# Kernel optimization log

Hardware: AMD Instinct MI355X
Metric: run time of the kernel (lower is better)

Reference implementation:

```python
import jax, jax.numpy as jnp
import numpy as np

N, E, H, C = 100000, 1600000, 4, 32  # nodes, edges, heads, per-head channels
F_IN, F_HID, F_OUT = 128, 32, 16
NEG_SLOPE = 0.2


def setup_inputs() -> dict:
    key = jax.random.key(0)
    ks = jax.random.split(key, 16)
    s = 0.05
    return {
        "x": jax.random.normal(ks[0], (N, F_IN), jnp.float32),
        "edge_index": jax.random.randint(ks[1], (2, E), 0, N, jnp.int32),
        "W0": jax.random.normal(ks[2], (F_IN, H * C), jnp.float32) * s,
        "att_src0": jax.random.normal(ks[3], (H, C), jnp.float32) * s,
        "att_dst0": jax.random.normal(ks[4], (H, C), jnp.float32) * s,
        "b0": jax.random.normal(ks[5], (H * C,), jnp.float32) * s,
        "W1": jax.random.normal(ks[6], (H * C, H * C), jnp.float32) * s,
        "att_src1": jax.random.normal(ks[7], (H, C), jnp.float32) * s,
        "att_dst1": jax.random.normal(ks[8], (H, C), jnp.float32) * s,
        "b1": jax.random.normal(ks[9], (H * C,), jnp.float32) * s,
        "Wm1": jax.random.normal(ks[10], (H * C, F_HID), jnp.float32) * s,
        "bm1": jax.random.normal(ks[11], (F_HID,), jnp.float32) * s,
        "Wm2": jax.random.normal(ks[12], (F_HID, F_OUT), jnp.float32) * s,
        "bm2": jax.random.normal(ks[13], (F_OUT,), jnp.float32) * s,
    }


def gat_layer(x, src, dst, W, att_src, att_dst, bias):
    n = x.shape[0]
    h = (x @ W).reshape(n, H, C)                       # [N,H,C]
    a_src = jnp.einsum("nhc,hc->nh", h, att_src)       # [N,H]
    a_dst = jnp.einsum("nhc,hc->nh", h, att_dst)       # [N,H]
    e = a_src[src] + a_dst[dst]                        # [E,H]
    e = jnp.where(e > 0, e, NEG_SLOPE * e)             # leaky_relu(0.2)
    m = jax.ops.segment_max(e, dst, num_segments=n)    # [N,H] segment softmax
    ee = jnp.exp(e - m[dst])
    z = jax.ops.segment_sum(ee, dst, num_segments=n)
    alpha = ee / z[dst]                                # [E,H]
    msg = alpha[:, :, None] * h[src]                   # [E,H,C]
    out = jax.ops.segment_sum(msg, dst, num_segments=n)  # [N,H,C]
    return out.reshape(n, H * C) + bias


def reference(x, edge_index, W0, att_src0, att_dst0, b0,
              W1, att_src1, att_dst1, b1, Wm1, bm1, Wm2, bm2):
    src, dst = edge_index[0], edge_index[1]
    x = jax.nn.relu(gat_layer(x, src, dst, W0, att_src0, att_dst0, b0))
    x = jax.nn.relu(gat_layer(x, src, dst, W1, att_src1, att_dst1, b1))
    x = jax.nn.relu(x @ Wm1 + bm1)
    return x @ Wm2 + bm2
```

## Files before the change

### kernel.cpp

```cpp
#include <hip/hip_runtime.h>
#include <hip/hip_bf16.h>

#define NEG 0.2f

typedef __attribute__((ext_vector_type(8))) short short8v;
typedef __attribute__((ext_vector_type(4))) float f32x4;

static __device__ __forceinline__ float bf2f(unsigned int u16){
  return __uint_as_float(u16 << 16);
}
static __device__ __forceinline__ unsigned short f2bf(float f){
  __hip_bfloat16 h = __float2bfloat16(f);
  return *reinterpret_cast<unsigned short*>(&h);
}

#define CHUNK 2048
#define PER_T 8


static __device__ __forceinline__ void bcount_body(
    const int* __restrict__ dst, int* __restrict__ bcnt, int E, int NB,
    int blk, int* lc)
{
  int t = threadIdx.x;
  int ebase = blk * CHUNK;
  for (int j=t; j<NB; j+=256) lc[j]=0;
  __syncthreads();
  #pragma unroll
  for (int k=0;k<PER_T;++k){
    int i = ebase + t + k*256;
    if (i < E) atomicAdd(&lc[dst[i] >> 8], 1);
  }
  __syncthreads();
  for (int j=t; j<NB; j+=256){
    int c = lc[j];
    if (c) atomicAdd(&bcnt[j], c);
  }
}

static __device__ __forceinline__ void binpass_body(
    const int* __restrict__ src, const int* __restrict__ dst,
    int* __restrict__ bfill, unsigned int* __restrict__ pairs, int E, int NB,
    int blk, int* lcnt, int* lbase)
{
  int t = threadIdx.x;
  int ebase = blk * CHUNK;
  for (int j=t; j<NB; j+=256) lcnt[j]=0;
  __syncthreads();
  unsigned int pv[PER_T]; int pb[PER_T];
  #pragma unroll
  for (int k=0;k<PER_T;++k){
    int i = ebase + t + k*256;
    pb[k] = -1;
    if (i < E){
      int d = dst[i];
      int s = src[i];
      pb[k] = d >> 8;
      pv[k] = ((unsigned int)s << 8) | (unsigned int)(d & 255);
      atomicAdd(&lcnt[pb[k]], 1);
    }
  }
  __syncthreads();
  for (int j=t; j<NB; j+=256){
    int c = lcnt[j];
    lbase[j] = c ? atomicAdd(&bfill[j], c) : 0;
    lcnt[j] = 0;
  }
  __syncthreads();
  #pragma unroll
  for (int k=0;k<PER_T;++k){
    if (pb[k] >= 0){
      int ofs = atomicAdd(&lcnt[pb[k]], 1);
      pairs[lbase[pb[k]] + ofs] = pv[k];
    }
  }
}

template<int IN_BF16>
static __device__ __forceinline__ void gemm_att_body(
    const void* __restrict__ xin_, const unsigned short* __restrict__ wt,
    const float* __restrict__ atts, const float* __restrict__ attd,
    unsigned short* __restrict__ hb, float* __restrict__ as_, float* __restrict__ ad_,
    int n, int blk, unsigned short* xls)
{
  int t = threadIdx.x;
  int base = blk*64;
  int nrem = n - base;
  if (IN_BF16){
    const uint4* Xb = reinterpret_cast<const uint4*>(xin_);
    #pragma unroll
    for (int j=0;j<4;++j){
      int i = t + j*256;
      int row = i >> 4, c16 = i & 15;
      uint4 v = (row < nrem) ? Xb[(size_t)(base+row)*16 + c16]
                             : make_uint4(0,0,0,0);
      int addr = row*256 + ((c16*16) ^ ((row&7)<<4));
      *reinterpret_cast<uint4*>(reinterpret_cast<char*>(xls) + addr) = v;
    }
  } else {
    const float4* X4 = reinterpret_cast<const float4*>(xin_);
    #pragma unroll
    for (int j=0;j<8;++j){
      int i = t + j*256;
      int row = i >> 5, cb = i & 31;
      float4 v = (row < nrem) ? X4[(size_t)(base+row)*32 + cb] : make_float4(0.f,0.f,0.f,0.f);
      unsigned int p0 = (unsigned int)f2bf(v.x) | ((unsigned int)f2bf(v.y)<<16);
      unsigned int p1 = (unsigned int)f2bf(v.z) | ((unsigned int)f2bf(v.w)<<16);
      int addr = row*256 + ((cb*8) ^ ((row&7)<<4));
      *reinterpret_cast<uint2*>(reinterpret_cast<char*>(xls) + addr) = make_uint2(p0,p1);
    }
  }
  __syncthreads();
  int w = t >> 6;
  int l = t & 63;
  int l15 = l & 15, l4 = l >> 4;
  int n0 = w*32;
  short8v bfr[2][4];
  #pragma unroll
  for (int nt=0;nt<2;++nt){
    const unsigned short* bp = wt + (size_t)(n0 + nt*16 + l15)*128 + l4*8;
    #pragma unroll
    for (int kk=0;kk<4;++kk)
      bfr[nt][kk] = *reinterpret_cast<const short8v*>(bp + kk*32);
  }
  f32x4 acc[4][2];
  #pragma unroll
  for (int mt=0;mt<4;++mt)
    #pragma unroll
    for (int nt=0;nt<2;++nt)
      acc[mt][nt] = (f32x4){0.f,0.f,0.f,0.f};
  #pragma unroll
  for (int kk=0;kk<4;++kk){
    short8v afr[4];
    #pragma unroll
    for (int mt=0;mt<4;++mt){
      int row = mt*16 + l15;
      int addr = row*256 + ((kk*64 + l4*16) ^ ((row&7)<<4));
      afr[mt] = *reinterpret_cast<const short8v*>(reinterpret_cast<char*>(xls) + addr);
    }
    #pragma unroll
    for (int mt=0;mt<4;++mt)
      #pragma unroll
      for (int nt=0;nt<2;++nt)
        acc[mt][nt] = __builtin_amdgcn_mfma_f32_16x16x32_bf16(afr[mt], bfr[nt][kk], acc[mt][nt], 0, 0, 0);
  }
  float av0 = atts[n0 + l15],    av1 = atts[n0 + 16 + l15];
  float dv0 = attd[n0 + l15],    dv1 = attd[n0 + 16 + l15];
  #pragma unroll
  for (int mt=0;mt<4;++mt){
    #pragma unroll
    for (int r=0;r<4;++r){
      float ps = acc[mt][0][r]*av0 + acc[mt][1][r]*av1;
      float pd = acc[mt][0][r]*dv0 + acc[mt][1][r]*dv1;
      ps += __shfl_xor(ps,1); ps += __shfl_xor(ps,2);
      ps += __shfl_xor(ps,4); ps += __shfl_xor(ps,8);
      pd += __shfl_xor(pd,1); pd += __shfl_xor(pd,2);
      pd += __shfl_xor(pd,4); pd += __shfl_xor(pd,8);
      int node = base + mt*16 + l4*4 + r;
      if (l15==0 && node < n){
        as_[node*4 + w] = ps;
        ad_[node*4 + w] = pd;
      }
    }
  }
  __syncthreads();
  #pragma unroll
  for (int mt=0;mt<4;++mt)
    #pragma unroll
    for (int nt=0;nt<2;++nt)
      #pragma unroll
      for (int r=0;r<4;++r){
        int row = mt*16 + l4*4 + r;
        int col = n0 + nt*16 + l15;
        xls[row*128 + col] = f2bf(acc[mt][nt][r]);
      }
  __syncthreads();
  const uint4* xsrc = reinterpret_cast<const uint4*>(xls);
  uint4* hdst = reinterpret_cast<uint4*>(hb + (size_t)base*128);
  #pragma unroll
  for (int j=0;j<4;++j){
    int i = t + j*256;
    int row = i >> 4;
    if (row < nrem) hdst[i] = xsrc[i];
  }
}


__global__ __launch_bounds__(256) void k_wconv_bcount(
    const float* __restrict__ W0, const float* __restrict__ W1,
    unsigned short* __restrict__ wt0, unsigned short* __restrict__ wt1,
    const int* __restrict__ dst, int* __restrict__ bcnt, int E, int NB)
{
  __shared__ int lc[512];
  int b = blockIdx.x;
  if (b < 128){
    const float* W = (b < 64) ? W0 : W1;
    unsigned short* wt = (b < 64) ? wt0 : wt1;
    int i = (b & 63)*256 + threadIdx.x;
    int k = i >> 7, nn = i & 127;
    wt[nn*128 + k] = f2bf(W[i]);
  } else {
    bcount_body(dst, bcnt, E, NB, b - 128, lc);
  }
}

__global__ __launch_bounds__(256) void k_bscan(
    const int* __restrict__ bcnt, int* __restrict__ bstart,
    int* __restrict__ bfill, int NB)
{
  __shared__ int sd[256];
  int t = threadIdx.x;
  int i0 = 2*t, i1 = 2*t+1;
  int v0 = (i0<NB) ? bcnt[i0] : 0;
  int v1 = (i1<NB) ? bcnt[i1] : 0;
  int s = v0+v1;
  sd[t]=s; __syncthreads();
  for (int off=1; off<256; off<<=1){
    int x = (t>=off) ? sd[t-off] : 0;
    __syncthreads();
    sd[t] += x;
    __syncthreads();
  }
  int ex = sd[t]-s;
  if (i0<=NB){ bstart[i0]=ex; if(i0<NB) bfill[i0]=ex; }
  ex += v0;
  if (i1<=NB){ bstart[i1]=ex; if(i1<NB) bfill[i1]=ex; }
}

__global__ __launch_bounds__(256) void k_gemm1_binpass(
    const float* __restrict__ xin, const unsigned short* __restrict__ wt,
    const float* __restrict__ atts, const float* __restrict__ attd,
    unsigned short* __restrict__ hb, float* __restrict__ as_, float* __restrict__ ad_,
    int n, int nBin,
    const int* __restrict__ src, const int* __restrict__ dst,
    int* __restrict__ bfill, unsigned int* __restrict__ pairs, int E, int NB)
{
  __shared__ __align__(16) unsigned short xls[64*128];
  __shared__ int lcnt[512];
  __shared__ int lbase[512];
  int b = blockIdx.x;
  if (b < nBin){
    binpass_body(src, dst, bfill, pairs, E, NB, b, lcnt, lbase);
  } else {
    gemm_att_body<0>(xin, wt, atts, attd, hb, as_, ad_, n, b - nBin, xls);
  }
}

__global__ __launch_bounds__(256) void k_gemm2(
    const unsigned short* __restrict__ xin, const unsigned short* __restrict__ wt,
    const float* __restrict__ atts, const float* __restrict__ attd,
    unsigned short* __restrict__ hb, float* __restrict__ as_, float* __restrict__ ad_, int n)
{
  __shared__ __align__(16) unsigned short xls[64*128];
  gemm_att_body<1>(xin, wt, atts, attd, hb, as_, ad_, n, blockIdx.x, xls);
}

__global__ __launch_bounds__(256) void k_csr(
    const unsigned int* __restrict__ pairs, const int* __restrict__ bstart,
    int* __restrict__ rowptr, int* __restrict__ csr, int n)
{
  __shared__ int lc[256];
  __shared__ int sd[256];
  __shared__ int rp[257];
  int b = blockIdx.x;
  int base = b << 8;
  int t = threadIdx.x;
  int cnt = n - base; if (cnt > 256) cnt = 256;
  int beg = bstart[b], end = bstart[b+1];
  lc[t]=0; __syncthreads();
  for (int i = beg + t; i < end; i += 256)
    atomicAdd(&lc[pairs[i] & 255u], 1);
  __syncthreads();
  int v = lc[t];
  sd[t]=v; __syncthreads();
  for (int off=1; off<256; off<<=1){
    int x = (t>=off) ? sd[t-off] : 0;
    __syncthreads();
    sd[t] += x;
    __syncthreads();
  }
  rp[t+1] = beg + sd[t];
  if (t==0) rp[0] = beg;
  lc[t] = 0;
  __syncthreads();
  if (t < cnt) rowptr[base + t] = rp[t];
  if (t==0 && base + cnt == n) rowptr[n] = rp[cnt];
  for (int i = beg + t; i < end; i += 256){
    unsigned int p = pairs[i];
    int d = (int)(p & 255u);
    int ofs = atomicAdd(&lc[d], 1);
    csr[rp[d] + ofs] = (int)(p >> 8);
  }
}

__global__ __launch_bounds__(256) void k_aggr(
    const unsigned short* __restrict__ hb, const float* __restrict__ as_,
    const float* __restrict__ ad_, const int* __restrict__ rowptr,
    const int* __restrict__ csr, const float* __restrict__ bias,
    unsigned short* __restrict__ out, int n)
{
  int wid = (int)((blockIdx.x*(size_t)blockDim.x + threadIdx.x) >> 6);
  int lane = threadIdx.x & 63;
  if (wid >= n) return;
  int half = lane >> 5;
  int li   = lane & 31;
  int c0   = li*4;
  int head = li >> 3;
  const uint2* __restrict__ h2 = reinterpret_cast<const uint2*>(hb);
  float adn = ad_[wid*4 + head];
  int beg = rowptr[wid], end = rowptr[wid+1];
  int deg = end - beg;
  float4 acc = make_float4(0.f,0.f,0.f,0.f);
  float z = 0.f;
  int nfull = deg & ~7;
  int lim = beg + nfull;
  int i = beg + half*4;
  int s0=0,s1=0,s2=0,s3=0;
  if (i < lim){ s0=csr[i]; s1=csr[i+1]; s2=csr[i+2]; s3=csr[i+3]; }
  for (; i < lim; ){
    int ni = i + 8;
    int t0=0,t1=0,t2=0,t3=0;
    if (ni < lim){ t0=csr[ni]; t1=csr[ni+1]; t2=csr[ni+2]; t3=csr[ni+3]; }
    float e0 = as_[s0*4+head];
    float e1 = as_[s1*4+head];
    float e2 = as_[s2*4+head];
    float e3 = as_[s3*4+head];
    uint2 p0 = h2[s0*32 + li];
    uint2 p1 = h2[s1*32 + li];
    uint2 p2 = h2[s2*32 + li];
    uint2 p3 = h2[s3*32 + li];
    e0 += adn; e1 += adn; e2 += adn; e3 += adn;
    e0 = (e0>0.f)?e0:NEG*e0;
    e1 = (e1>0.f)?e1:NEG*e1;
    e2 = (e2>0.f)?e2:NEG*e2;
    e3 = (e3>0.f)?e3:NEG*e3;
    float x0 = __expf(e0);
    float x1 = __expf(e1);
    float x2 = __expf(e2);
    float x3 = __expf(e3);
    z += (x0+x1)+(x2+x3);
    acc.x = fmaf(x0, bf2f(p0.x & 0xffffu), acc.x);
    acc.y = fmaf(x0, bf2f(p0.x >> 16),     acc.y);
    acc.z = fmaf(x0, bf2f(p0.y & 0xffffu), acc.z);
    acc.w = fmaf(x0, bf2f(p0.y >> 16),     acc.w);
    acc.x = fmaf(x1, bf2f(p1.x & 0xffffu), acc.x);
    acc.y = fmaf(x1, bf2f(p1.x >> 16),     acc.y);
    acc.z = fmaf(x1, bf2f(p1.y & 0xffffu), acc.z);
    acc.w = fmaf(x1, bf2f(p1.y >> 16),     acc.w);
    acc.x = fmaf(x2, bf2f(p2.x & 0xffffu), acc.x);
    acc.y = fmaf(x2, bf2f(p2.x >> 16),     acc.y);
    acc.z = fmaf(x2, bf2f(p2.y & 0xffffu), acc.z);
    acc.w = fmaf(x2, bf2f(p2.y >> 16),     acc.w);
    acc.x = fmaf(x3, bf2f(p3.x & 0xffffu), acc.x);
    acc.y = fmaf(x3, bf2f(p3.x >> 16),     acc.y);
    acc.z = fmaf(x3, bf2f(p3.y & 0xffffu), acc.z);
    acc.w = fmaf(x3, bf2f(p3.y >> 16),     acc.w);
    i = ni; s0=t0; s1=t1; s2=t2; s3=t3;
  }
  for (int j = beg + nfull + half; j < end; j += 2){
    int s = csr[j];
    float e = as_[s*4+head] + adn;
    e = (e>0.f)?e:NEG*e;
    float ee = __expf(e);
    z += ee;
    uint2 pv = h2[s*32 + li];
    acc.x = fmaf(ee, bf2f(pv.x & 0xffffu), acc.x);
    acc.y = fmaf(ee, bf2f(pv.x >> 16),     acc.y);
    acc.z = fmaf(ee, bf2f(pv.y & 0xffffu), acc.z);
    acc.w = fmaf(ee, bf2f(pv.y >> 16),     acc.w);
  }
  z     += __shfl_xor(z, 32);
  acc.x += __shfl_xor(acc.x, 32);
  acc.y += __shfl_xor(acc.y, 32);
  acc.z += __shfl_xor(acc.z, 32);
  acc.w += __shfl_xor(acc.w, 32);
  if (half == 0){
    float4 o;
    if (deg > 0){
      float rz = 1.f/z;
      o.x = fmaxf(fmaf(acc.x,rz,bias[c0  ]), 0.f);
      o.y = fmaxf(fmaf(acc.y,rz,bias[c0+1]), 0.f);
      o.z = fmaxf(fmaf(acc.z,rz,bias[c0+2]), 0.f);
      o.w = fmaxf(fmaf(acc.w,rz,bias[c0+3]), 0.f);
    } else {
      o.x = fmaxf(bias[c0  ], 0.f);
      o.y = fmaxf(bias[c0+1], 0.f);
      o.z = fmaxf(bias[c0+2], 0.f);
      o.w = fmaxf(bias[c0+3], 0.f);
    }
    unsigned int lo = (unsigned int)f2bf(o.x) | ((unsigned int)f2bf(o.y)<<16);
    unsigned int hi = (unsigned int)f2bf(o.z) | ((unsigned int)f2bf(o.w)<<16);
    *reinterpret_cast<uint2*>(out + (size_t)wid*128 + c0) = make_uint2(lo,hi);
  }
}

__global__ __launch_bounds__(256) void k_mlp(
    const unsigned short* __restrict__ xb, const float* __restrict__ Wm1, const float* __restrict__ bm1,
    const float* __restrict__ Wm2, const float* __restrict__ bm2,
    float* __restrict__ out, int n)
{
  __shared__ float xs[64*129];
  __shared__ float w1s[128*32];
  __shared__ float hs[64*33];
  __shared__ float w2s[32*16];
  __shared__ float b1s[32];
  __shared__ float b2s[16];
  int t = threadIdx.x;
  int base = blockIdx.x*64;
  const uint4* Xb = reinterpret_cast<const uint4*>(xb);
  #pragma unroll
  for (int j=0;j<4;++j){
    int i = t + j*256;
    int row = i >> 4, seg = i & 15;
    uint4 v = (base+row < n) ? Xb[(size_t)(base+row)*16 + seg] : make_uint4(0,0,0,0);
    float* xp = &xs[row*129 + seg*8];
    xp[0] = bf2f(v.x & 0xffffu); xp[1] = bf2f(v.x >> 16);
    xp[2] = bf2f(v.y & 0xffffu); xp[3] = bf2f(v.y >> 16);
    xp[4] = bf2f(v.z & 0xffffu); xp[5] = bf2f(v.z >> 16);
    xp[6] = bf2f(v.w & 0xffffu); xp[7] = bf2f(v.w >> 16);
  }
  for (int i=t; i<128*32; i+=256) w1s[i]=Wm1[i];
  for (int i=t; i<32*16;  i+=256) w2s[i]=Wm2[i];
  if (t<32) b1s[t]=bm1[t];
  if (t<16) b2s[t]=bm2[t];
  __syncthreads();
  int l = t&63, g = t>>6;
  float hid[8];
  #pragma unroll
  for (int j=0;j<8;++j) hid[j]=0.f;
  for (int k=0;k<128;++k){
    float xk = xs[l*129+k];
    #pragma unroll
    for (int j=0;j<8;++j) hid[j] = fmaf(xk, w1s[k*32 + g*8 + j], hid[j]);
  }
  #pragma unroll
  for (int j=0;j<8;++j) hs[l*33 + g*8 + j] = fmaxf(hid[j] + b1s[g*8+j], 0.f);
  __syncthreads();
  float o[4] = {0.f,0.f,0.f,0.f};
  for (int k=0;k<32;++k){
    float xv = hs[l*33+k];
    #pragma unroll
    for (int j=0;j<4;++j) o[j] = fmaf(xv, w2s[k*16 + g*4 + j], o[j]);
  }
  int node = base + l;
  if (node < n){
    #pragma unroll
    for (int j=0;j<4;++j) out[(size_t)node*16 + g*4 + j] = o[j] + b2s[g*4+j];
  }
}

extern "C" void kernel_launch(void* const* d_in, const int* in_sizes, int n_in,
                              void* d_out, int out_size, void* d_ws, size_t ws_size,
                              hipStream_t stream)
{
  const float* x   = (const float*)d_in[0];
  const int*   ei  = (const int*)  d_in[1];
  const float* W0  = (const float*)d_in[2];
  const float* as0 = (const float*)d_in[3];
  const float* ad0 = (const float*)d_in[4];
  const float* b0  = (const float*)d_in[5];
  const float* W1  = (const float*)d_in[6];
  const float* as1 = (const float*)d_in[7];
  const float* ad1 = (const float*)d_in[8];
  const float* b1  = (const float*)d_in[9];
  const float* Wm1 = (const float*)d_in[10];
  const float* bm1 = (const float*)d_in[11];
  const float* Wm2 = (const float*)d_in[12];
  const float* bm2 = (const float*)d_in[13];
  int N = in_sizes[0]/128;
  int E = in_sizes[1]/2;
  const int* srcI = ei;
  const int* dstI = ei + E;

  char* ws = (char*)d_ws;
  size_t off = 0;
  auto alloc = [&](size_t bytes)->void*{
    void* p = ws + off; off += (bytes + 255) & ~(size_t)255; return p;
  };
  unsigned short* hbuf = (unsigned short*)alloc((size_t)N*128*2);
  unsigned short* xbuf = (unsigned short*)alloc((size_t)N*128*2);
  float* asb   = (float*)alloc((size_t)N*4*4);
  float* adb   = (float*)alloc((size_t)N*4*4);
  int* rowptr  = (int*)alloc((size_t)(N+1)*4);
  int* bcnt    = (int*)alloc(2048);
  int* bstart  = (int*)alloc(2052);
  int* bfill   = (int*)alloc(2048);
  int* csr     = (int*)alloc((size_t)E*4);
  unsigned int* pairs = (unsigned int*)alloc((size_t)E*4);
  unsigned short* wt0 = (unsigned short*)alloc(128*128*2);
  unsigned short* wt1 = (unsigned short*)alloc(128*128*2);
  (void)ws_size; (void)n_in; (void)out_size;

  int NB = (N + 255) >> 8;
  int gC = (E + CHUNK - 1) / CHUNK;
  int gG = (N+63)/64;
  int gA = (int)(((size_t)N*64 + 255)/256);

  hipMemsetAsync(bcnt, 0, 2048, stream);
  k_wconv_bcount<<<128+gC,256,0,stream>>>(W0, W1, wt0, wt1, dstI, bcnt, E, NB);
  k_bscan       <<<1,256,0,stream>>>(bcnt, bstart, bfill, NB);
  k_gemm1_binpass<<<gG+gC,256,0,stream>>>(x, wt0, as0, ad0, hbuf, asb, adb, N, gC,
                                          srcI, dstI, bfill, pairs, E, NB);
  k_csr         <<<NB,256,0,stream>>>(pairs, bstart, rowptr, csr, N);
  k_aggr        <<<gA,256,0,stream>>>(hbuf, asb, adb, rowptr, csr, b0, xbuf, N);
  k_gemm2       <<<gG,256,0,stream>>>(xbuf, wt1, as1, ad1, hbuf, asb, adb, N);
  k_aggr        <<<gA,256,0,stream>>>(hbuf, asb, adb, rowptr, csr, b1, xbuf, N);
  k_mlp         <<<gG,256,0,stream>>>(xbuf, Wm1, bm1, Wm2, bm2, (float*)d_out, N);
}
```

Before: 294.5 us.

## Fuse bin scan into count kernel, use half-wave per node in aggregation

The bin-count kernel now has its last-finishing block, found through an atomic done counter, run the exclusive scan. This removes the separate single-block scan launch. The aggregation kernel maps one 32-lane group per node instead of a full 64-lane wave split into halves, which drops the cross-half shuffle reduction and the idle half-wave on low-degree nodes. Row pointers are stored as int2 (begin,end) pairs so each node needs one load. GEMM blocks are also placed first in the combined gemm/binpass launch. The tradeoff is a longer serial edge loop per lane group and reliance on threadfence plus atomic ordering for the last-block scan.

```diff
diff --git a/kernel.cpp b/kernel.cpp
--- a/kernel.cpp
+++ b/kernel.cpp
@@ -17,26 +17,6 @@
 #define CHUNK 2048
 #define PER_T 8
 
-
-static __device__ __forceinline__ void bcount_body(
-    const int* __restrict__ dst, int* __restrict__ bcnt, int E, int NB,
-    int blk, int* lc)
-{
-  int t = threadIdx.x;
-  int ebase = blk * CHUNK;
-  for (int j=t; j<NB; j+=256) lc[j]=0;
-  __syncthreads();
-  #pragma unroll
-  for (int k=0;k<PER_T;++k){
-    int i = ebase + t + k*256;
-    if (i < E) atomicAdd(&lc[dst[i] >> 8], 1);
-  }
-  __syncthreads();
-  for (int j=t; j<NB; j+=256){
-    int c = lc[j];
-    if (c) atomicAdd(&bcnt[j], c);
-  }
-}
 
 static __device__ __forceinline__ void binpass_body(
     const int* __restrict__ src, const int* __restrict__ dst,
@@ -189,39 +169,52 @@
 __global__ __launch_bounds__(256) void k_wconv_bcount(
     const float* __restrict__ W0, const float* __restrict__ W1,
     unsigned short* __restrict__ wt0, unsigned short* __restrict__ wt1,
-    const int* __restrict__ dst, int* __restrict__ bcnt, int E, int NB)
+    const int* __restrict__ dst, int* __restrict__ bcnt,
+    int* __restrict__ bstart, int* __restrict__ bfill, int* __restrict__ done,
+    int E, int NB, int nBc)
 {
   __shared__ int lc[512];
+  __shared__ int amLast;
   int b = blockIdx.x;
+  int t = threadIdx.x;
   if (b < 128){
     const float* W = (b < 64) ? W0 : W1;
     unsigned short* wt = (b < 64) ? wt0 : wt1;
-    int i = (b & 63)*256 + threadIdx.x;
+    int i = (b & 63)*256 + t;
     int k = i >> 7, nn = i & 127;
     wt[nn*128 + k] = f2bf(W[i]);
-  } else {
-    bcount_body(dst, bcnt, E, NB, b - 128, lc);
-  }
-}
-
-__global__ __launch_bounds__(256) void k_bscan(
-    const int* __restrict__ bcnt, int* __restrict__ bstart,
-    int* __restrict__ bfill, int NB)
-{
-  __shared__ int sd[256];
-  int t = threadIdx.x;
+    return;
+  }
+  int blk = b - 128;
+  int ebase = blk * CHUNK;
+  for (int j=t; j<NB; j+=256) lc[j]=0;
+  __syncthreads();
+  #pragma unroll
+  for (int k=0;k<PER_T;++k){
+    int i = ebase + t + k*256;
+    if (i < E) atomicAdd(&lc[dst[i] >> 8], 1);
+  }
+  __syncthreads();
+  for (int j=t; j<NB; j+=256){
+    int c = lc[j];
+    if (c) atomicAdd(&bcnt[j], c);
+  }
+  __threadfence();
+  if (t==0) amLast = (atomicAdd(done, 1) == nBc-1) ? 1 : 0;
+  __syncthreads();
+  if (!amLast) return;
   int i0 = 2*t, i1 = 2*t+1;
-  int v0 = (i0<NB) ? bcnt[i0] : 0;
-  int v1 = (i1<NB) ? bcnt[i1] : 0;
+  int v0 = (i0<NB) ? atomicAdd(&bcnt[i0],0) : 0;
+  int v1 = (i1<NB) ? atomicAdd(&bcnt[i1],0) : 0;
   int s = v0+v1;
-  sd[t]=s; __syncthreads();
+  lc[t]=s; __syncthreads();
   for (int off=1; off<256; off<<=1){
-    int x = (t>=off) ? sd[t-off] : 0;
+    int x = (t>=off) ? lc[t-off] : 0;
     __syncthreads();
-    sd[t] += x;
+    lc[t] += x;
     __syncthreads();
   }
-  int ex = sd[t]-s;
+  int ex = lc[t]-s;
   if (i0<=NB){ bstart[i0]=ex; if(i0<NB) bfill[i0]=ex; }
   ex += v0;
   if (i1<=NB){ bstart[i1]=ex; if(i1<NB) bfill[i1]=ex; }
@@ -231,7 +224,7 @@
     const float* __restrict__ xin, const unsigned short* __restrict__ wt,
     const float* __restrict__ atts, const float* __restrict__ attd,
     unsigned short* __restrict__ hb, float* __restrict__ as_, float* __restrict__ ad_,
-    int n, int nBin,
+    int n, int nG,
     const int* __restrict__ src, const int* __restrict__ dst,
     int* __restrict__ bfill, unsigned int* __restrict__ pairs, int E, int NB)
 {
@@ -239,10 +232,10 @@
   __shared__ int lcnt[512];
   __shared__ int lbase[512];
   int b = blockIdx.x;
-  if (b < nBin){
-    binpass_body(src, dst, bfill, pairs, E, NB, b, lcnt, lbase);
+  if (b < nG){
+    gemm_att_body<0>(xin, wt, atts, attd, hb, as_, ad_, n, b, xls);
   } else {
-    gemm_att_body<0>(xin, wt, atts, attd, hb, as_, ad_, n, b - nBin, xls);
+    binpass_body(src, dst, bfill, pairs, E, NB, b - nG, lcnt, lbase);
   }
 }
 
@@ -257,7 +250,7 @@
 
 __global__ __launch_bounds__(256) void k_csr(
     const unsigned int* __restrict__ pairs, const int* __restrict__ bstart,
-    int* __restrict__ rowptr, int* __restrict__ csr, int n)
+    int2* __restrict__ rp2, int* __restrict__ csr, int n)
 {
   __shared__ int lc[256];
   __shared__ int sd[256];
@@ -283,8 +276,7 @@
   if (t==0) rp[0] = beg;
   lc[t] = 0;
   __syncthreads();
-  if (t < cnt) rowptr[base + t] = rp[t];
-  if (t==0 && base + cnt == n) rowptr[n] = rp[cnt];
+  if (t < cnt) rp2[base + t] = make_int2(rp[t], rp[t+1]);
   for (int i = beg + t; i < end; i += 256){
     unsigned int p = pairs[i];
     int d = (int)(p & 255u);
@@ -295,30 +287,29 @@
 
 __global__ __launch_bounds__(256) void k_aggr(
     const unsigned short* __restrict__ hb, const float* __restrict__ as_,
-    const float* __restrict__ ad_, const int* __restrict__ rowptr,
+    const float* __restrict__ ad_, const int2* __restrict__ rp2,
     const int* __restrict__ csr, const float* __restrict__ bias,
     unsigned short* __restrict__ out, int n)
 {
-  int wid = (int)((blockIdx.x*(size_t)blockDim.x + threadIdx.x) >> 6);
-  int lane = threadIdx.x & 63;
-  if (wid >= n) return;
-  int half = lane >> 5;
-  int li   = lane & 31;
-  int c0   = li*4;
+  int node = (int)((blockIdx.x*(size_t)blockDim.x + threadIdx.x) >> 5);
+  int li = threadIdx.x & 31;
+  if (node >= n) return;
+  int c0 = li*4;
   int head = li >> 3;
   const uint2* __restrict__ h2 = reinterpret_cast<const uint2*>(hb);
-  float adn = ad_[wid*4 + head];
-  int beg = rowptr[wid], end = rowptr[wid+1];
+  float adn = ad_[node*4 + head];
+  int2 be = rp2[node];
+  int beg = be.x, end = be.y;
   int deg = end - beg;
   float4 acc = make_float4(0.f,0.f,0.f,0.f);
   float z = 0.f;
-  int nfull = deg & ~7;
+  int nfull = deg & ~3;
   int lim = beg + nfull;
-  int i = beg + half*4;
+  int i = beg;
   int s0=0,s1=0,s2=0,s3=0;
   if (i < lim){ s0=csr[i]; s1=csr[i+1]; s2=csr[i+2]; s3=csr[i+3]; }
   for (; i < lim; ){
-    int ni = i + 8;
+    int ni = i + 4;
     int t0=0,t1=0,t2=0,t3=0;
     if (ni < lim){ t0=csr[ni]; t1=csr[ni+1]; t2=csr[ni+2]; t3=csr[ni+3]; }
     float e0 = as_[s0*4+head];
@@ -357,7 +348,7 @@
     acc.w = fmaf(x3, bf2f(p3.y >> 16),     acc.w);
     i = ni; s0=t0; s1=t1; s2=t2; s3=t3;
   }
-  for (int j = beg + nfull + half; j < end; j += 2){
+  for (int j = beg + nfull; j < end; ++j){
     int s = csr[j];
     float e = as_[s*4+head] + adn;
     e = (e>0.f)?e:NEG*e;
@@ -369,29 +360,22 @@
     acc.z = fmaf(ee, bf2f(pv.y & 0xffffu), acc.z);
     acc.w = fmaf(ee, bf2f(pv.y >> 16),     acc.w);
   }
-  z     += __shfl_xor(z, 32);
-  acc.x += __shfl_xor(acc.x, 32);
-  acc.y += __shfl_xor(acc.y, 32);
-  acc.z += __shfl_xor(acc.z, 32);
-  acc.w += __shfl_xor(acc.w, 32);
-  if (half == 0){
-    float4 o;
-    if (deg > 0){
-      float rz = 1.f/z;
-      o.x = fmaxf(fmaf(acc.x,rz,bias[c0  ]), 0.f);
-      o.y = fmaxf(fmaf(acc.y,rz,bias[c0+1]), 0.f);
-      o.z = fmaxf(fmaf(acc.z,rz,bias[c0+2]), 0.f);
-      o.w = fmaxf(fmaf(acc.w,rz,bias[c0+3]), 0.f);
-    } else {
-      o.x = fmaxf(bias[c0  ], 0.f);
-      o.y = fmaxf(bias[c0+1], 0.f);
-      o.z = fmaxf(bias[c0+2], 0.f);
-      o.w = fmaxf(bias[c0+3], 0.f);
-    }
-    unsigned int lo = (unsigned int)f2bf(o.x) | ((unsigned int)f2bf(o.y)<<16);
-    unsigned int hi = (unsigned int)f2bf(o.z) | ((unsigned int)f2bf(o.w)<<16);
-    *reinterpret_cast<uint2*>(out + (size_t)wid*128 + c0) = make_uint2(lo,hi);
-  }
+  float4 o;
+  if (deg > 0){
+    float rz = 1.f/z;
+    o.x = fmaxf(fmaf(acc.x,rz,bias[c0  ]), 0.f);
+    o.y = fmaxf(fmaf(acc.y,rz,bias[c0+1]), 0.f);
+    o.z = fmaxf(fmaf(acc.z,rz,bias[c0+2]), 0.f);
+    o.w = fmaxf(fmaf(acc.w,rz,bias[c0+3]), 0.f);
+  } else {
+    o.x = fmaxf(bias[c0  ], 0.f);
+    o.y = fmaxf(bias[c0+1], 0.f);
+    o.z = fmaxf(bias[c0+2], 0.f);
+    o.w = fmaxf(bias[c0+3], 0.f);
+  }
+  unsigned int lo = (unsigned int)f2bf(o.x) | ((unsigned int)f2bf(o.y)<<16);
+  unsigned int hi = (unsigned int)f2bf(o.z) | ((unsigned int)f2bf(o.w)<<16);
+  reinterpret_cast<uint2*>(out)[node*32 + li] = make_uint2(lo,hi);
 }
 
 __global__ __launch_bounds__(256) void k_mlp(
@@ -481,8 +465,8 @@
   unsigned short* xbuf = (unsigned short*)alloc((size_t)N*128*2);
   float* asb   = (float*)alloc((size_t)N*4*4);
   float* adb   = (float*)alloc((size_t)N*4*4);
-  int* rowptr  = (int*)alloc((size_t)(N+1)*4);
-  int* bcnt    = (int*)alloc(2048);
+  int2* rp2    = (int2*)alloc((size_t)N*8);
+  int* bcnt    = (int*)alloc(2304);
   int* bstart  = (int*)alloc(2052);
   int* bfill   = (int*)alloc(2048);
   int* csr     = (int*)alloc((size_t)E*4);
@@ -490,20 +474,21 @@
   unsigned short* wt0 = (unsigned short*)alloc(128*128*2);
   unsigned short* wt1 = (unsigned short*)alloc(128*128*2);
   (void)ws_size; (void)n_in; (void)out_size;
+  int* done = bcnt + 512;
 
   int NB = (N + 255) >> 8;
   int gC = (E + CHUNK - 1) / CHUNK;
   int gG = (N+63)/64;
-  int gA = (int)(((size_t)N*64 + 255)/256);
-
-  hipMemsetAsync(bcnt, 0, 2048, stream);
-  k_wconv_bcount<<<128+gC,256,0,stream>>>(W0, W1, wt0, wt1, dstI, bcnt, E, NB);
-  k_bscan       <<<1,256,0,stream>>>(bcnt, bstart, bfill, NB);
-  k_gemm1_binpass<<<gG+gC,256,0,stream>>>(x, wt0, as0, ad0, hbuf, asb, adb, N, gC,
+  int gA = (int)(((size_t)N*32 + 255)/256);
+
+  hipMemsetAsync(bcnt, 0, 2304, stream);
+  k_wconv_bcount<<<128+gC,256,0,stream>>>(W0, W1, wt0, wt1, dstI, bcnt,
+                                          bstart, bfill, done, E, NB, gC);
+  k_gemm1_binpass<<<gG+gC,256,0,stream>>>(x, wt0, as0, ad0, hbuf, asb, adb, N, gG,
                                           srcI, dstI, bfill, pairs, E, NB);
-  k_csr         <<<NB,256,0,stream>>>(pairs, bstart, rowptr, csr, N);
-  k_aggr        <<<gA,256,0,stream>>>(hbuf, asb, adb, rowptr, csr, b0, xbuf, N);
+  k_csr         <<<NB,256,0,stream>>>(pairs, bstart, rp2, csr, N);
+  k_aggr        <<<gA,256,0,stream>>>(hbuf, asb, adb, rp2, csr, b0, xbuf, N);
   k_gemm2       <<<gG,256,0,stream>>>(xbuf, wt1, as1, ad1, hbuf, asb, adb, N);
-  k_aggr        <<<gA,256,0,stream>>>(hbuf, asb, adb, rowptr, csr, b1, xbuf, N);
+  k_aggr        <<<gA,256,0,stream>>>(hbuf, asb, adb, rp2, csr, b1, xbuf, N);
   k_mlp         <<<gG,256,0,stream>>>(xbuf, Wm1, bm1, Wm2, bm2, (float*)d_out, N);
 }
```

Measured after the change: 320.5 us. 1.09x slower.
